# Optimization experiments

Hardware: AMD Instinct MI355X
Metric: run time of the kernel (lower is better)

The kernel has to match this reference:

```python
import jax, jax.numpy as jnp
import numpy as np

N = 100000          # num nodes
E = 3200000         # num edges (avg degree 32)
G = 64              # num graphs in batch
F_IN = 2            # num_node_features
H = 16              # hidden_size
NUM_LAYERS = 2


def sage_conv(x, src, dst, W_l, b_l, W_r):
    # PyG SAGEConv (mean aggr): out = lin_l(mean_{j in N(i)} x_j) + lin_r(x_i)
    msg = x[src]                                                  # [E, F] gather
    agg = jax.ops.segment_sum(msg, dst, num_segments=N)          # [N, F] scatter-add
    deg = jax.ops.segment_sum(jnp.ones((src.shape[0],), x.dtype), dst, num_segments=N)
    mean = agg / jnp.maximum(deg, 1.0)[:, None]
    return mean @ W_l + b_l + x @ W_r


def setup_inputs() -> dict:
    key = jax.random.key(0)
    ks = jax.random.split(key, 10)
    x = jax.random.normal(ks[0], (N, F_IN), dtype=jnp.float32)
    edge_index = jax.random.randint(ks[1], (2, E), 0, N, dtype=jnp.int64)
    batch = jnp.sort(jax.random.randint(ks[2], (N,), 0, G, dtype=jnp.int64))
    s1 = 1.0 / np.sqrt(F_IN)
    s2 = 1.0 / np.sqrt(H)
    return {
        "x": x,
        "edge_index": edge_index,
        "batch": batch,
        "W1_l": jax.random.uniform(ks[3], (F_IN, H), jnp.float32, -s1, s1),
        "b1_l": jnp.zeros((H,), jnp.float32),
        "W1_r": jax.random.uniform(ks[4], (F_IN, H), jnp.float32, -s1, s1),
        "W2_l": jax.random.uniform(ks[5], (H, H), jnp.float32, -s2, s2),
        "b2_l": jnp.zeros((H,), jnp.float32),
        "W2_r": jax.random.uniform(ks[6], (H, H), jnp.float32, -s2, s2),
        "W_end": jax.random.uniform(ks[7], (H, 1), jnp.float32, -s2, s2),
        "b_end": jnp.zeros((1,), jnp.float32),
    }


def reference(x, edge_index, batch, W1_l, b1_l, W1_r, W2_l, b2_l, W2_r, W_end, b_end):
    src, dst = edge_index[0], edge_index[1]
    h = sage_conv(x, src, dst, W1_l, b1_l, W1_r)                 # conv1
    for _ in range(NUM_LAYERS - 1):
        h = jax.nn.relu(h)
        h = sage_conv(h, src, dst, W2_l, b2_l, W2_r)             # conv2
    h = jax.nn.relu(h)
    # dropout is identity in eval mode
    h = h @ W_end + b_end                                         # [N, 1]
    # global mean pool over graphs
    summed = jax.ops.segment_sum(h, batch, num_segments=G)       # [G, 1]
    counts = jax.ops.segment_sum(jnp.ones((N,), h.dtype), batch, num_segments=G)
    pooled = summed / jnp.maximum(counts, 1.0)[:, None]
    return jax.nn.sigmoid(pooled)                                 # [G, 1]
```

## Files before the change

### kernel.cpp

```cpp
#include <hip/hip_runtime.h>
#include <math.h>

#define NN 100000
#define NE 3200000
#define NG 64
#define HID 16
#define EPB 8192
#define NBLKE ((NE + EPB - 1) / EPB)
#define NBUCK ((NN + 255) / 256)
#define LMAX 10240

typedef unsigned int uint;
typedef float vf2 __attribute__((ext_vector_type(2)));


template <bool HI>
__device__ inline vf2 dec2fp8(uint u) {
#if __has_builtin(__builtin_amdgcn_cvt_pk_f32_fp8)
    return __builtin_amdgcn_cvt_pk_f32_fp8((int)u, HI);
#else
    vf2 r;
    uint b0 = (u >> (HI ? 16 : 0)) & 0xff;
    uint b1 = (u >> (HI ? 24 : 8)) & 0xff;
    uint em0 = b0 & 0x7f, em1 = b1 & 0x7f;
    float v0 = (em0 >= 8) ? __uint_as_float(((em0 >> 3) + 120) << 23 | (em0 & 7) << 20)
                          : (float)em0 * 0.001953125f;
    float v1 = (em1 >= 8) ? __uint_as_float(((em1 >> 3) + 120) << 23 | (em1 & 7) << 20)
                          : (float)em1 * 0.001953125f;
    r.x = (b0 & 0x80) ? -v0 : v0;
    r.y = (b1 & 0x80) ? -v1 : v1;
    return r;
#endif
}

__device__ inline uint enc1fp8(float f) {
    if (!(f > 0.f)) return 0u;
    f = fminf(f, 448.f);
    uint b = __float_as_uint(f);
    int e = (int)(b >> 23) - 127;
    if (e >= -6) {
        uint m = b & 0x7fffffu;
        uint r = (m + 0x7ffffu + ((m >> 20) & 1u)) >> 20;
        uint code = ((uint)(e + 7) << 3) + r;
        return code > 126u ? 126u : code;
    }
    float t = f * 512.f;
    return (uint)(t + 0.5f);
}

template <bool HI>
__device__ inline uint packfp8x2(float a, float b, uint old) {
#if __has_builtin(__builtin_amdgcn_cvt_pk_fp8_f32)
    return (uint)__builtin_amdgcn_cvt_pk_fp8_f32(a, b, (int)old, HI);
#else
    uint v = enc1fp8(a) | (enc1fp8(b) << 8);
    return HI ? ((old & 0x0000ffffu) | (v << 16)) : ((old & 0xffff0000u) | v);
#endif
}

__global__ __launch_bounds__(512) void k_bhist(const int* __restrict__ dst,
                                               int* __restrict__ blockCnt) {
    __shared__ int h[NBUCK];
    int t = threadIdx.x;
    for (int i = t; i < NBUCK; i += 512) h[i] = 0;
    __syncthreads();
    int base = blockIdx.x * EPB;
    int n4 = (min(base + EPB, NE) - base) >> 2;
    const int4* d4 = (const int4*)(dst + base);
    for (int i = t; i < n4; i += 512) {
        int4 v = d4[i];
        atomicAdd(&h[v.x >> 8], 1);
        atomicAdd(&h[v.y >> 8], 1);
        atomicAdd(&h[v.z >> 8], 1);
        atomicAdd(&h[v.w >> 8], 1);
    }
    __syncthreads();
    for (int i = t; i < NBUCK; i += 512)
        blockCnt[i * NBLKE + blockIdx.x] = h[i];
}

__global__ __launch_bounds__(512) void k_bucketscan(int* __restrict__ blockCnt,
                                                    int* __restrict__ bucketTot) {
    __shared__ int a[512];
    int t = threadIdx.x, b = blockIdx.x;
    a[t] = (t < NBLKE) ? blockCnt[b * NBLKE + t] : 0;
    __syncthreads();
    for (int off = 1; off < 512; off <<= 1) {
        int x = a[t] + ((t >= off) ? a[t - off] : 0);
        __syncthreads();
        a[t] = x;
        __syncthreads();
    }
    if (t < NBLKE) blockCnt[b * NBLKE + t] = (t ? a[t - 1] : 0);
    if (t == 0) bucketTot[b] = a[511];
}

__global__ __launch_bounds__(512) void k_basescan(const int* __restrict__ bucketTot,
                                                  int* __restrict__ bucketBase,
                                                  int* __restrict__ offs,
                                                  float* __restrict__ gsum,
                                                  float* __restrict__ gcnt) {
    __shared__ int a[512];
    int t = threadIdx.x;
    if (t < NG) { gsum[t] = 0.f; gcnt[t] = 0.f; }
    a[t] = (t < NBUCK) ? bucketTot[t] : 0;
    __syncthreads();
    for (int off = 1; off < 512; off <<= 1) {
        int x = a[t] + ((t >= off) ? a[t - off] : 0);
        __syncthreads();
        a[t] = x;
        __syncthreads();
    }
    if (t < NBUCK) bucketBase[t] = (t ? a[t - 1] : 0);
    if (t == 0) { bucketBase[NBUCK] = a[511]; offs[NN] = a[511]; }
}

__global__ __launch_bounds__(512) void k_bscatter(const int* __restrict__ src,
                                                  const int* __restrict__ dst,
                                                  const int* __restrict__ blockCnt,
                                                  const int* __restrict__ bucketBase,
                                                  int* __restrict__ pairs) {
    __shared__ int cur[NBUCK];
    int t = threadIdx.x;
    for (int i = t; i < NBUCK; i += 512)
        cur[i] = blockCnt[i * NBLKE + blockIdx.x] + bucketBase[i];
    __syncthreads();
    int base = blockIdx.x * EPB;
    int n4 = (min(base + EPB, NE) - base) >> 2;
    const int4* d4 = (const int4*)(dst + base);
    const int4* s4 = (const int4*)(src + base);
    for (int i = t; i < n4; i += 512) {
        int4 dv = d4[i];
        int4 sv = s4[i];
        int p0 = atomicAdd(&cur[dv.x >> 8], 1);
        pairs[p0] = (sv.x << 8) | (dv.x & 255);
        int p1 = atomicAdd(&cur[dv.y >> 8], 1);
        pairs[p1] = (sv.y << 8) | (dv.y & 255);
        int p2 = atomicAdd(&cur[dv.z >> 8], 1);
        pairs[p2] = (sv.z << 8) | (dv.z & 255);
        int p3 = atomicAdd(&cur[dv.w >> 8], 1);
        pairs[p3] = (sv.w << 8) | (dv.w & 255);
    }
}

__global__ __launch_bounds__(512) void k_fill2c1(
    const int* __restrict__ bucketBase, const int* __restrict__ pairs,
    const float* __restrict__ x,
    const float* __restrict__ W1l, const float* __restrict__ b1l,
    const float* __restrict__ W1r,
    int* __restrict__ offs, int* __restrict__ csr, uint* __restrict__ h8) {
    __shared__ int a[256];
    __shared__ int lcur[256];
    __shared__ int lss[LMAX];
    int t = threadIdx.x, b = blockIdx.x;
    int pb = bucketBase[b], pe = bucketBase[b + 1];
    if (t < 256) a[t] = 0;
    __syncthreads();
    for (int e = pb + t; e < pe; e += 512)
        atomicAdd(&a[pairs[e] & 255], 1);
    __syncthreads();
    for (int off = 1; off < 256; off <<= 1) {
        int v = 0;
        if (t < 256) v = a[t] + ((t >= off) ? a[t - off] : 0);
        __syncthreads();
        if (t < 256) a[t] = v;
        __syncthreads();
    }
    if (t < 256) lcur[t] = t ? a[t - 1] : 0;
    __syncthreads();
    for (int e = pb + t; e < pe; e += 512) {
        int v = pairs[e];
        int s = v >> 8, dl = v & 255;
        int lpos = atomicAdd(&lcur[dl], 1);
        csr[pb + lpos] = s;
        if (lpos < LMAX) lss[lpos] = s;
    }
    __syncthreads();
    if (t < 256) {
        int node = b * 256 + t;
        if (node < NN) {
            int excl = t ? a[t - 1] : 0;
            int cntn = a[t] - excl;
            offs[node] = pb + excl;
            float s0 = 0.f, s1 = 0.f;
            for (int k = 0; k < cntn; ++k) {
                int idx = excl + k;
                int s = (idx < LMAX) ? lss[idx] : csr[pb + idx];
                float2 xv = *(const float2*)(x + 2 * s);
                s0 += xv.x; s1 += xv.y;
            }
            float inv = 1.0f / fmaxf((float)cntn, 1.0f);
            float m0 = s0 * inv, m1 = s1 * inv;
            float x0 = x[2 * node], x1 = x[2 * node + 1];
            float o[16];
#pragma unroll
            for (int h = 0; h < 16; ++h)
                o[h] = fmaxf(m0 * W1l[h] + m1 * W1l[16 + h] + b1l[h]
                           + x0 * W1r[h] + x1 * W1r[16 + h], 0.f);
            uint4 w;
            w.x = packfp8x2<false>(o[0],  o[1],  0u);
            w.x = packfp8x2<true >(o[2],  o[3],  w.x);
            w.y = packfp8x2<false>(o[4],  o[5],  0u);
            w.y = packfp8x2<true >(o[6],  o[7],  w.y);
            w.z = packfp8x2<false>(o[8],  o[9],  0u);
            w.z = packfp8x2<true >(o[10], o[11], w.z);
            w.w = packfp8x2<false>(o[12], o[13], 0u);
            w.w = packfp8x2<true >(o[14], o[15], w.w);
            *(uint4*)(h8 + (size_t)node * 4) = w;
        }
    }
}

__global__ __launch_bounds__(256) void k_conv2pool(
    const int* __restrict__ offs, const int* __restrict__ csr,
    const uint* __restrict__ h8,
    const float* __restrict__ W2l, const float* __restrict__ b2l,
    const float* __restrict__ W2r, const float* __restrict__ Wend,
    const float* __restrict__ bend, const int* __restrict__ batch,
    float* __restrict__ gsum, float* __restrict__ gcnt) {
    __shared__ float sWl[256], sWr[256], sB[HID], sWe[HID];
    __shared__ float sm[64][17], shr[64][17];
    __shared__ float ls[NG], lc[NG];
    int t = threadIdx.x;
    sWl[t] = W2l[t];
    sWr[t] = W2r[t];
    if (t < HID) { sB[t] = b2l[t]; sWe[t] = Wend[t]; }
    if (t < NG) { ls[t] = 0.f; lc[t] = 0.f; }

    int g = t >> 2;
    int l4 = t & 3;
    int gbase = (t & 63) & 60;
    int i = blockIdx.x * 64 + g;
    int beg = 0, end = 0;
    if (i < NN) { beg = offs[i]; end = offs[i + 1]; }
    float a0 = 0.f, a1 = 0.f, a2 = 0.f, a3 = 0.f;
    int kb = beg;
    uint ub[8];
    for (; kb + 8 <= end; kb += 8) {
        int sv0 = csr[kb + l4];
        int sv1 = csr[kb + 4 + l4];
#pragma unroll
        for (int j = 0; j < 4; ++j) {
            int s = __shfl(sv0, gbase + j, 64);
            ub[j] = h8[(size_t)s * 4 + l4];
        }
#pragma unroll
        for (int j = 0; j < 4; ++j) {
            int s = __shfl(sv1, gbase + j, 64);
            ub[4 + j] = h8[(size_t)s * 4 + l4];
        }
#pragma unroll
        for (int j = 0; j < 8; ++j) {
            vf2 p0 = dec2fp8<false>(ub[j]);
            vf2 p1 = dec2fp8<true >(ub[j]);
            a0 += p0.x; a1 += p0.y; a2 += p1.x; a3 += p1.y;
        }
    }
    for (; kb + 4 <= end; kb += 4) {
        int sv = csr[kb + l4];
#pragma unroll
        for (int j = 0; j < 4; ++j) {
            int s = __shfl(sv, gbase + j, 64);
            ub[j] = h8[(size_t)s * 4 + l4];
        }
#pragma unroll
        for (int j = 0; j < 4; ++j) {
            vf2 p0 = dec2fp8<false>(ub[j]);
            vf2 p1 = dec2fp8<true >(ub[j]);
            a0 += p0.x; a1 += p0.y; a2 += p1.x; a3 += p1.y;
        }
    }
    if (kb < end) {
        int idx = kb + l4;
        int sv = (idx < end) ? csr[idx] : 0;
        int nb = end - kb;
        for (int j = 0; j < nb; ++j) {
            int s = __shfl(sv, gbase + j, 64);
            uint u = h8[(size_t)s * 4 + l4];
            vf2 p0 = dec2fp8<false>(u);
            vf2 p1 = dec2fp8<true >(u);
            a0 += p0.x; a1 += p0.y; a2 += p1.x; a3 += p1.y;
        }
    }
    if (i < NN) {
        float inv = 1.0f / fmaxf((float)(end - beg), 1.0f);
        uint us = h8[(size_t)i * 4 + l4];
        vf2 q0 = dec2fp8<false>(us);
        vf2 q1 = dec2fp8<true >(us);
        sm[g][4 * l4 + 0] = a0 * inv;
        sm[g][4 * l4 + 1] = a1 * inv;
        sm[g][4 * l4 + 2] = a2 * inv;
        sm[g][4 * l4 + 3] = a3 * inv;
        shr[g][4 * l4 + 0] = q0.x;
        shr[g][4 * l4 + 1] = q0.y;
        shr[g][4 * l4 + 2] = q1.x;
        shr[g][4 * l4 + 3] = q1.y;
    }
    __syncthreads();

    float y = 0.f;
    if (i < NN) {
#pragma unroll
        for (int k = 0; k < 4; ++k) {
            int h = 4 * l4 + k;
            float a = sB[h];
#pragma unroll
            for (int f = 0; f < HID; ++f)
                a += sm[g][f] * sWl[f * HID + h] + shr[g][f] * sWr[f * HID + h];
            y += fmaxf(a, 0.f) * sWe[h];
        }
    }
    y += __shfl_xor(y, 1, 64);
    y += __shfl_xor(y, 2, 64);
    if (l4 == 0 && i < NN) {
        int bg = batch[i];
        atomicAdd(&ls[bg], y + bend[0]);
        atomicAdd(&lc[bg], 1.0f);
    }
    __syncthreads();
    if (t < NG && lc[t] != 0.0f) {
        unsafeAtomicAdd(&gsum[t], ls[t]);
        unsafeAtomicAdd(&gcnt[t], lc[t]);
    }
}

__global__ void k_final(const float* __restrict__ gsum, const float* __restrict__ gcnt,
                        float* __restrict__ out) {
    int g = threadIdx.x;
    if (g < NG) {
        float p = gsum[g] / fmaxf(gcnt[g], 1.0f);
        out[g] = 1.0f / (1.0f + expf(-p));
    }
}

extern "C" void kernel_launch(void* const* d_in, const int* in_sizes, int n_in,
                              void* d_out, int out_size, void* d_ws, size_t ws_size,
                              hipStream_t stream) {
    const float* x    = (const float*)d_in[0];
    const int*   ei   = (const int*)d_in[1];
    const int*   batch= (const int*)d_in[2];
    const float* W1l  = (const float*)d_in[3];
    const float* b1l  = (const float*)d_in[4];
    const float* W1r  = (const float*)d_in[5];
    const float* W2l  = (const float*)d_in[6];
    const float* b2l  = (const float*)d_in[7];
    const float* W2r  = (const float*)d_in[8];
    const float* Wend = (const float*)d_in[9];
    const float* bend = (const float*)d_in[10];

    const int* src = ei;
    const int* dst = ei + NE;

    float* gsum      = (float*)d_ws;
    float* gcnt      = (float*)d_ws + NG;
    int*   blockCnt  = (int*)d_ws + 2 * NG;
    int*   bucketTot = blockCnt + (size_t)NBLKE * NBUCK;
    int*   bucketBase= bucketTot + NBUCK;
    int*   offs      = bucketBase + NBUCK + 1;
    size_t po        = (size_t)(offs - (int*)d_ws) + NN + 1;
    po               = (po + 3) & ~(size_t)3;
    int*   pairs     = (int*)d_ws + po;
    int*   csr       = pairs + NE;
    uint*  h8        = (uint*)(csr + NE);

    k_bhist     <<<NBLKE, 512, 0, stream>>>(dst, blockCnt);
    k_bucketscan<<<NBUCK, 512, 0, stream>>>(blockCnt, bucketTot);
    k_basescan  <<<1, 512, 0, stream>>>(bucketTot, bucketBase, offs, gsum, gcnt);
    k_bscatter  <<<NBLKE, 512, 0, stream>>>(src, dst, blockCnt, bucketBase, pairs);
    k_fill2c1   <<<NBUCK, 512, 0, stream>>>(bucketBase, pairs, x, W1l, b1l, W1r,
                                            offs, csr, h8);
    k_conv2pool <<<(NN + 63) / 64, 256, 0, stream>>>(offs, csr, h8, W2l, b2l, W2r,
                                                     Wend, bend, batch, gsum, gcnt);
    k_final     <<<1, 64, 0, stream>>>(gsum, gcnt, (float*)d_out);
}
```

Baseline: 105.5 us.

## Use nontemporal loads/stores, split conv1 gather across all threads, fuse final kernel

Result: slower. 385.3 us (+265.4%).

```diff
diff --git a/kernel.cpp b/kernel.cpp
--- a/kernel.cpp
+++ b/kernel.cpp
@@ -12,6 +12,7 @@
 
 typedef unsigned int uint;
 typedef float vf2 __attribute__((ext_vector_type(2)));
+typedef int   vi4 __attribute__((ext_vector_type(4)));
 
 
 template <bool HI>
@@ -66,9 +67,9 @@
     __syncthreads();
     int base = blockIdx.x * EPB;
     int n4 = (min(base + EPB, NE) - base) >> 2;
-    const int4* d4 = (const int4*)(dst + base);
+    const vi4* d4 = (const vi4*)(dst + base);
     for (int i = t; i < n4; i += 512) {
-        int4 v = d4[i];
+        vi4 v = __builtin_nontemporal_load(d4 + i);
         atomicAdd(&h[v.x >> 8], 1);
         atomicAdd(&h[v.y >> 8], 1);
         atomicAdd(&h[v.z >> 8], 1);
@@ -99,10 +100,12 @@
                                                   int* __restrict__ bucketBase,
                                                   int* __restrict__ offs,
                                                   float* __restrict__ gsum,
-                                                  float* __restrict__ gcnt) {
+                                                  float* __restrict__ gcnt,
+                                                  uint* __restrict__ done) {
     __shared__ int a[512];
     int t = threadIdx.x;
     if (t < NG) { gsum[t] = 0.f; gcnt[t] = 0.f; }
+    if (t == 0) *done = 0u;
     a[t] = (t < NBUCK) ? bucketTot[t] : 0;
     __syncthreads();
     for (int off = 1; off < 512; off <<= 1) {
@@ -127,19 +130,19 @@
     __syncthreads();
     int base = blockIdx.x * EPB;
     int n4 = (min(base + EPB, NE) - base) >> 2;
-    const int4* d4 = (const int4*)(dst + base);
-    const int4* s4 = (const int4*)(src + base);
+    const vi4* d4 = (const vi4*)(dst + base);
+    const vi4* s4 = (const vi4*)(src + base);
     for (int i = t; i < n4; i += 512) {
-        int4 dv = d4[i];
-        int4 sv = s4[i];
+        vi4 dv = __builtin_nontemporal_load(d4 + i);
+        vi4 sv = __builtin_nontemporal_load(s4 + i);
         int p0 = atomicAdd(&cur[dv.x >> 8], 1);
-        pairs[p0] = (sv.x << 8) | (dv.x & 255);
+        __builtin_nontemporal_store((sv.x << 8) | (dv.x & 255), pairs + p0);
         int p1 = atomicAdd(&cur[dv.y >> 8], 1);
-        pairs[p1] = (sv.y << 8) | (dv.y & 255);
+        __builtin_nontemporal_store((sv.y << 8) | (dv.y & 255), pairs + p1);
         int p2 = atomicAdd(&cur[dv.z >> 8], 1);
-        pairs[p2] = (sv.z << 8) | (dv.z & 255);
+        __builtin_nontemporal_store((sv.z << 8) | (dv.z & 255), pairs + p2);
         int p3 = atomicAdd(&cur[dv.w >> 8], 1);
-        pairs[p3] = (sv.w << 8) | (dv.w & 255);
+        __builtin_nontemporal_store((sv.w << 8) | (dv.w & 255), pairs + p3);
     }
 }
 
@@ -152,6 +155,7 @@
     __shared__ int a[256];
     __shared__ int lcur[256];
     __shared__ int lss[LMAX];
+    __shared__ float ps0[512], ps1[512];
     int t = threadIdx.x, b = blockIdx.x;
     int pb = bucketBase[b], pe = bucketBase[b + 1];
     if (t < 256) a[t] = 0;
@@ -169,11 +173,26 @@
     if (t < 256) lcur[t] = t ? a[t - 1] : 0;
     __syncthreads();
     for (int e = pb + t; e < pe; e += 512) {
-        int v = pairs[e];
+        int v = __builtin_nontemporal_load(pairs + e);
         int s = v >> 8, dl = v & 255;
         int lpos = atomicAdd(&lcur[dl], 1);
-        csr[pb + lpos] = s;
+        __builtin_nontemporal_store(s, csr + pb + lpos);
         if (lpos < LMAX) lss[lpos] = s;
+    }
+    __syncthreads();
+    {
+        int node8 = t & 255;
+        int half = t >> 8;
+        int excl = node8 ? a[node8 - 1] : 0;
+        int cntn = a[node8] - excl;
+        float s0 = 0.f, s1 = 0.f;
+        for (int k = half; k < cntn; k += 2) {
+            int idx = excl + k;
+            int s = (idx < LMAX) ? lss[idx] : csr[pb + idx];
+            float2 xv = *(const float2*)(x + 2 * s);
+            s0 += xv.x; s1 += xv.y;
+        }
+        ps0[t] = s0; ps1[t] = s1;
     }
     __syncthreads();
     if (t < 256) {
@@ -182,15 +201,9 @@
             int excl = t ? a[t - 1] : 0;
             int cntn = a[t] - excl;
             offs[node] = pb + excl;
-            float s0 = 0.f, s1 = 0.f;
-            for (int k = 0; k < cntn; ++k) {
-                int idx = excl + k;
-                int s = (idx < LMAX) ? lss[idx] : csr[pb + idx];
-                float2 xv = *(const float2*)(x + 2 * s);
-                s0 += xv.x; s1 += xv.y;
-            }
             float inv = 1.0f / fmaxf((float)cntn, 1.0f);
-            float m0 = s0 * inv, m1 = s1 * inv;
+            float m0 = (ps0[t] + ps0[t + 256]) * inv;
+            float m1 = (ps1[t] + ps1[t + 256]) * inv;
             float x0 = x[2 * node], x1 = x[2 * node + 1];
             float o[16];
 #pragma unroll
@@ -217,10 +230,12 @@
     const float* __restrict__ W2l, const float* __restrict__ b2l,
     const float* __restrict__ W2r, const float* __restrict__ Wend,
     const float* __restrict__ bend, const int* __restrict__ batch,
-    float* __restrict__ gsum, float* __restrict__ gcnt) {
+    float* __restrict__ gsum, float* __restrict__ gcnt,
+    uint* __restrict__ done, float* __restrict__ out) {
     __shared__ float sWl[256], sWr[256], sB[HID], sWe[HID];
     __shared__ float sm[64][17], shr[64][17];
     __shared__ float ls[NG], lc[NG];
+    __shared__ int lastBlock;
     int t = threadIdx.x;
     sWl[t] = W2l[t];
     sWr[t] = W2r[t];
@@ -237,8 +252,8 @@
     int kb = beg;
     uint ub[8];
     for (; kb + 8 <= end; kb += 8) {
-        int sv0 = csr[kb + l4];
-        int sv1 = csr[kb + 4 + l4];
+        int sv0 = __builtin_nontemporal_load(csr + kb + l4);
+        int sv1 = __builtin_nontemporal_load(csr + kb + 4 + l4);
 #pragma unroll
         for (int j = 0; j < 4; ++j) {
             int s = __shfl(sv0, gbase + j, 64);
@@ -257,7 +272,7 @@
         }
     }
     for (; kb + 4 <= end; kb += 4) {
-        int sv = csr[kb + l4];
+        int sv = __builtin_nontemporal_load(csr + kb + l4);
 #pragma unroll
         for (int j = 0; j < 4; ++j) {
             int s = __shfl(sv, gbase + j, 64);
@@ -272,7 +287,7 @@
     }
     if (kb < end) {
         int idx = kb + l4;
-        int sv = (idx < end) ? csr[idx] : 0;
+        int sv = (idx < end) ? __builtin_nontemporal_load(csr + idx) : 0;
         int nb = end - kb;
         for (int j = 0; j < nb; ++j) {
             int s = __shfl(sv, gbase + j, 64);
@@ -322,14 +337,18 @@
         unsafeAtomicAdd(&gsum[t], ls[t]);
         unsafeAtomicAdd(&gcnt[t], lc[t]);
     }
-}
-
-__global__ void k_final(const float* __restrict__ gsum, const float* __restrict__ gcnt,
-                        float* __restrict__ out) {
-    int g = threadIdx.x;
-    if (g < NG) {
-        float p = gsum[g] / fmaxf(gcnt[g], 1.0f);
-        out[g] = 1.0f / (1.0f + expf(-p));
+    __threadfence();
+    __syncthreads();
+    if (t == 0) {
+        uint old = atomicAdd(done, 1u);
+        lastBlock = (old == (uint)gridDim.x - 1);
+    }
+    __syncthreads();
+    if (lastBlock && t < NG) {
+        float s = unsafeAtomicAdd(&gsum[t], 0.0f);
+        float c = unsafeAtomicAdd(&gcnt[t], 0.0f);
+        float p = s / fmaxf(c, 1.0f);
+        out[t] = 1.0f / (1.0f + expf(-p));
     }
 }
 
@@ -353,7 +372,8 @@
 
     float* gsum      = (float*)d_ws;
     float* gcnt      = (float*)d_ws + NG;
-    int*   blockCnt  = (int*)d_ws + 2 * NG;
+    uint*  done      = (uint*)d_ws + 2 * NG;
+    int*   blockCnt  = (int*)d_ws + 2 * NG + 1;
     int*   bucketTot = blockCnt + (size_t)NBLKE * NBUCK;
     int*   bucketBase= bucketTot + NBUCK;
     int*   offs      = bucketBase + NBUCK + 1;
@@ -365,11 +385,11 @@
 
     k_bhist     <<<NBLKE, 512, 0, stream>>>(dst, blockCnt);
     k_bucketscan<<<NBUCK, 512, 0, stream>>>(blockCnt, bucketTot);
-    k_basescan  <<<1, 512, 0, stream>>>(bucketTot, bucketBase, offs, gsum, gcnt);
+    k_basescan  <<<1, 512, 0, stream>>>(bucketTot, bucketBase, offs, gsum, gcnt, done);
     k_bscatter  <<<NBLKE, 512, 0, stream>>>(src, dst, blockCnt, bucketBase, pairs);
     k_fill2c1   <<<NBUCK, 512, 0, stream>>>(bucketBase, pairs, x, W1l, b1l, W1r,
                                             offs, csr, h8);
     k_conv2pool <<<(NN + 63) / 64, 256, 0, stream>>>(offs, csr, h8, W2l, b2l, W2r,
-                                                     Wend, bend, batch, gsum, gcnt);
-    k_final     <<<1, 64, 0, stream>>>(gsum, gcnt, (float*)d_out);
-}
+                                                     Wend, bend, batch, gsum, gcnt,
+                                                     done, (float*)d_out);
+}
```
